# Kernel tuning notes

Measured on AMD Instinct MI355X. Metric: run time of the kernel, lower is better.

Reference implementation:

```python
import jax, jax.numpy as jnp
import numpy as np

B, P, N, E, H, D = 64, 256, 1000, 128, 8, 16
SQRT_E = 11.313708498984761  # sqrt(embedding_dim)
CLIP = 10.0                  # logit_clipping


def setup_inputs() -> dict:
    key = jax.random.key(0)
    ks = jax.random.split(key, 9)
    s = 0.05  # weight init scale
    return {
        "encoded_nodes": jax.random.normal(ks[0], (B, N, E), jnp.float32),
        "encoded_last_node": jax.random.normal(ks[1], (B, P, E), jnp.float32),
        "attr": jax.random.uniform(ks[2], (B, P, 1), jnp.float32),
        "ninf_mask": jnp.zeros((B, P, N), jnp.float32),
        # params stored [in, out] (apply as x @ W, equals torch Linear with W.T)
        "Wq_last": jax.random.normal(ks[3], (E + 1, H * D), jnp.float32) * s,
        "Wk": jax.random.normal(ks[4], (E, H * D), jnp.float32) * s,
        "Wv": jax.random.normal(ks[5], (E, H * D), jnp.float32) * s,
        "Wo": jax.random.normal(ks[6], (H * D, E), jnp.float32) * s,
        "bo": jax.random.normal(ks[7], (E,), jnp.float32) * s,
    }


def reference(encoded_nodes, encoded_last_node, attr, ninf_mask,
              Wq_last, Wk, Wv, Wo, bo):
    # set_kv: project encoded nodes to per-head K, V  -> [B, N, H, D]
    k = (encoded_nodes @ Wk).reshape(B, N, H, D)
    v = (encoded_nodes @ Wv).reshape(B, N, H, D)

    # query from (last node embedding, attr) -> [B, P, H, D]
    input_cat = jnp.concatenate([encoded_last_node, attr], axis=2)  # [B,P,E+1]
    q = (input_cat @ Wq_last).reshape(B, P, H, D)

    # multi-head attention with additive rank-3 -inf mask
    inv_sqrt_d = 1.0 / jnp.sqrt(jnp.float32(D))
    scores = jnp.einsum("bphd,bnhd->bhpn", q, k) * inv_sqrt_d
    scores = scores + ninf_mask[:, None, :, :]            # [B,H,P,N]
    weights = jax.nn.softmax(scores, axis=-1)
    out = jnp.einsum("bhpn,bnhd->bphd", weights, v).reshape(B, P, H * D)

    mh = out @ Wo + bo                                    # [B,P,E]

    # single-head tanh-clipped scoring against encoded nodes
    score = jnp.einsum("bpe,bne->bpn", mh, encoded_nodes) / SQRT_E
    score_masked = CLIP * jnp.tanh(score) + ninf_mask
    probs = jax.nn.softmax(score_masked, axis=2)          # [B,P,N]
    return probs
```

## Files before the change

kernel.cpp:

```cpp
#include <hip/hip_runtime.h>

#define BB 64
#define PP 256
#define NN 1000
#define NP 1024
#define EE 128
#define HH 8
#define DD 16

typedef __fp16 v4h __attribute__((ext_vector_type(4)));
typedef float v4f __attribute__((ext_vector_type(4)));


__global__ __launch_bounds__(256) void k1_qproj(const float* __restrict__ ln,
                                                const float* __restrict__ attr,
                                                const float* __restrict__ Wq,
                                                __fp16* __restrict__ Qh) {
    __shared__ __fp16 wt[128 * 132];
    __shared__ float attrs[64];
    const int tid = threadIdx.x;
    const int row0 = blockIdx.x * 64;
    for (int i = tid; i < 128 * 128; i += 256) {
        int k = i >> 7, n = i & 127;
        wt[n * 132 + k] = (__fp16)Wq[i];
    }
    if (tid < 64) attrs[tid] = attr[row0 + tid];
    __syncthreads();

    const int wid = tid >> 6, lane = tid & 63;
    const int lp = lane & 15, lg = lane >> 4;
    const int rb = row0 + wid * 16;

    const float* arow = ln + (size_t)(rb + lp) * 128;
    v4f acc[8];
#pragma unroll
    for (int cf = 0; cf < 8; cf++) acc[cf] = (v4f){0.f, 0.f, 0.f, 0.f};

#pragma unroll
    for (int k0 = 0; k0 < 8; k0++) {
        float4 av = *(const float4*)&arow[k0 * 16 + 4 * lg];
        v4h af;
        af[0] = (__fp16)av.x; af[1] = (__fp16)av.y;
        af[2] = (__fp16)av.z; af[3] = (__fp16)av.w;
#pragma unroll
        for (int cf = 0; cf < 8; cf++) {
            v4h bf = *(const v4h*)&wt[(cf * 16 + lp) * 132 + k0 * 16 + 4 * lg];
            acc[cf] = __builtin_amdgcn_mfma_f32_16x16x16f16(af, bf, acc[cf], 0, 0, 0);
        }
    }

#pragma unroll
    for (int cf = 0; cf < 8; cf++) {
        const int col = cf * 16 + lp;
        const float w128 = Wq[128 * 128 + col];
#pragma unroll
        for (int r = 0; r < 4; r++) {
            const int rl = wid * 16 + 4 * lg + r;
            float v = (acc[cf][r] + attrs[rl] * w128) * 0.25f;
            Qh[(size_t)(row0 + rl) * 128 + col] = (__fp16)v;
        }
    }
}

__global__ __launch_bounds__(256) void k2_kv(const float* __restrict__ nodes,
                                             const float* __restrict__ Wk,
                                             const float* __restrict__ Wv,
                                             __fp16* __restrict__ Kf,
                                             __fp16* __restrict__ Vt) {
    __shared__ __fp16 wt[128 * 132];
    const int tid = threadIdx.x;
    const int b = blockIdx.y;
    const int kv = blockIdx.z;
    const float* W = (kv == 0) ? Wk : Wv;
    for (int i = tid; i < 128 * 128; i += 256) {
        int k = i >> 7, n = i & 127;
        wt[n * 132 + k] = (__fp16)W[i];
    }
    __syncthreads();

    const int wid = tid >> 6, lane = tid & 63;
    const int lp = lane & 15, lg = lane >> 4;
    const int nb = blockIdx.x * 64 + wid * 16;

    int nr = nb + lp;
    if (nr >= NN) nr = NN - 1;
    const float* arow = nodes + (size_t)(b * NN + nr) * 128;

    v4f acc[8];
#pragma unroll
    for (int cf = 0; cf < 8; cf++) acc[cf] = (v4f){0.f, 0.f, 0.f, 0.f};

#pragma unroll
    for (int k0 = 0; k0 < 8; k0++) {
        float4 av = *(const float4*)&arow[k0 * 16 + 4 * lg];
        v4h af;
        af[0] = (__fp16)av.x; af[1] = (__fp16)av.y;
        af[2] = (__fp16)av.z; af[3] = (__fp16)av.w;
#pragma unroll
        for (int cf = 0; cf < 8; cf++) {
            v4h bf = *(const v4h*)&wt[(cf * 16 + lp) * 132 + k0 * 16 + 4 * lg];
            acc[cf] = __builtin_amdgcn_mfma_f32_16x16x16f16(af, bf, acc[cf], 0, 0, 0);
        }
    }

    if (kv == 0) {
#pragma unroll
        for (int cf = 0; cf < 8; cf++) {
            const size_t base = ((size_t)(b * HH + cf) << 14) + lp;
#pragma unroll
            for (int r = 0; r < 4; r++) {
                const int n = nb + 4 * lg + r;
                Kf[base + (size_t)n * 16] = (n < NN) ? (__fp16)acc[cf][r] : (__fp16)0.f;
            }
        }
    } else {
#pragma unroll
        for (int cf = 0; cf < 8; cf++) {
            v4h pk;
#pragma unroll
            for (int r = 0; r < 4; r++) {
                const int n = nb + 4 * lg + r;
                pk[r] = (n < NN) ? (__fp16)acc[cf][r] : (__fp16)0.f;
            }
            *(v4h*)&Vt[((size_t)(b * HH + cf) << 14) + (size_t)(nb >> 4) * 256 +
                       lp * 16 + 4 * lg] = pk;
        }
    }
}

__global__ __launch_bounds__(256) void k3_attn(const __fp16* __restrict__ Qh,
                                               const __fp16* __restrict__ Kf,
                                               const __fp16* __restrict__ Vt,
                                               const float* __restrict__ mask,
                                               __fp16* __restrict__ Aout) {
    __shared__ __fp16 sh[2][4][256];
    const int tid = threadIdx.x;
    const int bid = blockIdx.x;
    const int b = bid & 63;
    const int rest = bid >> 6;
    const int hg = rest & 3, pt = rest >> 2;
    const int h0 = hg * 2;
    const int p0 = pt * 64;

    const int wid = tid >> 6, lane = tid & 63;
    const int lp = lane & 15, lg = lane >> 4;
    const int pw = p0 + wid * 16;

    const __fp16* gsrc = ((wid < 2) ? Kf + ((size_t)(b * HH + h0 + wid) << 14)
                                    : Vt + ((size_t)(b * HH + h0 + wid - 2) << 14)) +
                         lane * 4;
    __fp16* sdst0 = &sh[0][wid][lane * 4];
    __fp16* sdst1 = &sh[1][wid][lane * 4];

    v4h qf[2];
    {
        const __fp16* qrow = Qh + (size_t)(b * PP + pw + lp) * 128 + h0 * 16 + 4 * lg;
        qf[0] = *(const v4h*)&qrow[0];
        qf[1] = *(const v4h*)&qrow[16];
    }

    const float* mrow = mask + (size_t)(b * PP + pw + lp) * NN;

    v4f acc[2];
    float lsum[2];
    acc[0] = (v4f){0.f, 0.f, 0.f, 0.f};
    acc[1] = (v4f){0.f, 0.f, 0.f, 0.f};
    lsum[0] = 0.f; lsum[1] = 0.f;
    const v4f zero4 = {0.f, 0.f, 0.f, 0.f};

    v4h st[2];
    float4 mv[2];
    st[0] = *(const v4h*)(gsrc);
    *(v4h*)sdst0 = st[0];
    st[1] = *(const v4h*)(gsrc + 256);
    mv[0] = *(const float4*)&mrow[4 * lg];
    __syncthreads();

#pragma unroll 2
    for (int s = 0; s < 62; s++) {
        const int p = s & 1;
        if (s + 2 <= 62) st[p] = *(const v4h*)(gsrc + (s + 2) * 256);
        {
            int moff = (s + 1) * 16 + 4 * lg;
            if (moff > 996) moff = 996;
            mv[p ^ 1] = *(const float4*)&mrow[moff];
        }

        v4h kf0 = *(const v4h*)&sh[p][0][lp * 16 + 4 * lg];
        v4h kf1 = *(const v4h*)&sh[p][1][lp * 16 + 4 * lg];
        v4h vf0 = *(const v4h*)&sh[p][2][lp * 16 + 4 * lg];
        v4h vf1 = *(const v4h*)&sh[p][3][lp * 16 + 4 * lg];
        const float4 m = mv[p];
        {
            v4f sc = __builtin_amdgcn_mfma_f32_16x16x16f16(kf0, qf[0], zero4, 0, 0, 0);
            float w0 = __expf(sc[0] + m.x);
            float w1 = __expf(sc[1] + m.y);
            float w2 = __expf(sc[2] + m.z);
            float w3 = __expf(sc[3] + m.w);
            lsum[0] += (w0 + w1) + (w2 + w3);
            v4h wf;
            wf[0] = (__fp16)w0; wf[1] = (__fp16)w1; wf[2] = (__fp16)w2; wf[3] = (__fp16)w3;
            acc[0] = __builtin_amdgcn_mfma_f32_16x16x16f16(wf, vf0, acc[0], 0, 0, 0);
        }
        {
            v4f sc = __builtin_amdgcn_mfma_f32_16x16x16f16(kf1, qf[1], zero4, 0, 0, 0);
            float w0 = __expf(sc[0] + m.x);
            float w1 = __expf(sc[1] + m.y);
            float w2 = __expf(sc[2] + m.z);
            float w3 = __expf(sc[3] + m.w);
            lsum[1] += (w0 + w1) + (w2 + w3);
            v4h wf;
            wf[0] = (__fp16)w0; wf[1] = (__fp16)w1; wf[2] = (__fp16)w2; wf[3] = (__fp16)w3;
            acc[1] = __builtin_amdgcn_mfma_f32_16x16x16f16(wf, vf1, acc[1], 0, 0, 0);
        }

        *(v4h*)((p == 0) ? sdst1 : sdst0) = st[p ^ 1];
        __syncthreads();
    }

    {
        const int nl = 992;
        const float4 m = mv[0];
        const bool c0 = (nl + 4 * lg + 0 < NN), c1 = (nl + 4 * lg + 1 < NN);
        const bool c2 = (nl + 4 * lg + 2 < NN), c3 = (nl + 4 * lg + 3 < NN);
        v4h kf0 = *(const v4h*)&sh[0][0][lp * 16 + 4 * lg];
        v4h kf1 = *(const v4h*)&sh[0][1][lp * 16 + 4 * lg];
        v4h vf0 = *(const v4h*)&sh[0][2][lp * 16 + 4 * lg];
        v4h vf1 = *(const v4h*)&sh[0][3][lp * 16 + 4 * lg];
        {
            v4f sc = __builtin_amdgcn_mfma_f32_16x16x16f16(kf0, qf[0], zero4, 0, 0, 0);
            float w0 = c0 ? __expf(sc[0] + m.x) : 0.f;
            float w1 = c1 ? __expf(sc[1] + m.y) : 0.f;
            float w2 = c2 ? __expf(sc[2] + m.z) : 0.f;
            float w3 = c3 ? __expf(sc[3] + m.w) : 0.f;
            lsum[0] += (w0 + w1) + (w2 + w3);
            v4h wf;
            wf[0] = (__fp16)w0; wf[1] = (__fp16)w1; wf[2] = (__fp16)w2; wf[3] = (__fp16)w3;
            acc[0] = __builtin_amdgcn_mfma_f32_16x16x16f16(wf, vf0, acc[0], 0, 0, 0);
        }
        {
            v4f sc = __builtin_amdgcn_mfma_f32_16x16x16f16(kf1, qf[1], zero4, 0, 0, 0);
            float w0 = c0 ? __expf(sc[0] + m.x) : 0.f;
            float w1 = c1 ? __expf(sc[1] + m.y) : 0.f;
            float w2 = c2 ? __expf(sc[2] + m.z) : 0.f;
            float w3 = c3 ? __expf(sc[3] + m.w) : 0.f;
            lsum[1] += (w0 + w1) + (w2 + w3);
            v4h wf;
            wf[0] = (__fp16)w0; wf[1] = (__fp16)w1; wf[2] = (__fp16)w2; wf[3] = (__fp16)w3;
            acc[1] = __builtin_amdgcn_mfma_f32_16x16x16f16(wf, vf1, acc[1], 0, 0, 0);
        }
    }

#pragma unroll
    for (int j = 0; j < 2; j++) {
        float l = lsum[j];
        l += __shfl_xor(l, 16);
        l += __shfl_xor(l, 32);
#pragma unroll
        for (int r = 0; r < 4; r++) {
            float denom = __shfl(l, 4 * lg + r);
            float inv = 1.f / denom;
            Aout[(size_t)(b * PP + pw + 4 * lg + r) * 128 + (h0 + j) * 16 + lp] =
                (__fp16)(acc[j][r] * inv);
        }
    }
}

__global__ __launch_bounds__(256) void k4_mh(const __fp16* __restrict__ Ain,
                                             const float* __restrict__ Wo,
                                             const float* __restrict__ bo,
                                             __fp16* __restrict__ Mh) {
    __shared__ __fp16 wt[128 * 132];
    const int tid = threadIdx.x;
    const int row0 = blockIdx.x * 64;
    for (int i = tid; i < 128 * 128; i += 256) {
        int k = i >> 7, n = i & 127;
        wt[n * 132 + k] = (__fp16)Wo[i];
    }
    __syncthreads();

    const int wid = tid >> 6, lane = tid & 63;
    const int lp = lane & 15, lg = lane >> 4;
    const int rb = row0 + wid * 16;

    const __fp16* arow = Ain + (size_t)(rb + lp) * 128;
    v4f acc[8];
#pragma unroll
    for (int cf = 0; cf < 8; cf++) acc[cf] = (v4f){0.f, 0.f, 0.f, 0.f};

#pragma unroll
    for (int k0 = 0; k0 < 8; k0++) {
        v4h af = *(const v4h*)&arow[k0 * 16 + 4 * lg];
#pragma unroll
        for (int cf = 0; cf < 8; cf++) {
            v4h bf = *(const v4h*)&wt[(cf * 16 + lp) * 132 + k0 * 16 + 4 * lg];
            acc[cf] = __builtin_amdgcn_mfma_f32_16x16x16f16(af, bf, acc[cf], 0, 0, 0);
        }
    }

    const float scale = 0.08838834764831845f;
#pragma unroll
    for (int cf = 0; cf < 8; cf++) {
        const int col = cf * 16 + lp;
        const float bb = bo[col];
#pragma unroll
        for (int r = 0; r < 4; r++) {
            const int rl = wid * 16 + 4 * lg + r;
            Mh[(size_t)(row0 + rl) * 128 + col] = (__fp16)((acc[cf][r] + bb) * scale);
        }
    }
}

__device__ __forceinline__ void k5_pref(int s, int wid, int lp, int lg,
                                        const float* __restrict__ nbase,
                                        float4 (&nb)[8]) {
    int nr = s * 128 + wid * 16 + lp;
    if (nr >= NN) nr = NN - 1;
    const float* a = nbase + (size_t)nr * 128 + 4 * lg;
#pragma unroll
    for (int ec = 0; ec < 8; ec++) nb[ec] = *(const float4*)&a[ec * 16];
}

__device__ __forceinline__ void k5_comp(int s, int wid, int lp, int lg,
                                        const v4h (&bf0)[8], const v4h (&bf1)[8],
                                        const float4 (&nb)[8],
                                        const float* __restrict__ mk0,
                                        const float* __restrict__ mk1,
                                        float& ls0, float& ls1,
                                        __fp16* __restrict__ probs) {
    const v4f zero4 = {0.f, 0.f, 0.f, 0.f};
    int mc = s * 128 + wid * 16 + 4 * lg;
    if (mc > 996) mc = 996;
    float4 m0 = *(const float4*)&mk0[mc];
    float4 m1 = *(const float4*)&mk1[mc];
    v4f a0 = zero4, a1 = zero4;
#pragma unroll
    for (int ec = 0; ec < 8; ec++) {
        float4 av = nb[ec];
        v4h af;
        af[0] = (__fp16)av.x; af[1] = (__fp16)av.y;
        af[2] = (__fp16)av.z; af[3] = (__fp16)av.w;
        a0 = __builtin_amdgcn_mfma_f32_16x16x16f16(af, bf0[ec], a0, 0, 0, 0);
        a1 = __builtin_amdgcn_mfma_f32_16x16x16f16(af, bf1[ec], a1, 0, 0, 0);
    }
    const int nt = s * 128 + wid * 16;
    const int nb4 = nt + 4 * lg;
#pragma unroll
    for (int t = 0; t < 2; t++) {
        const v4f ac = t ? a1 : a0;
        const float4 m = t ? m1 : m0;
        v4h wf;
        float ws = 0.f;
        if (nt + 15 < NN) {
            float e0 = __expf(2.f * ac[0]);
            float e1 = __expf(2.f * ac[1]);
            float e2 = __expf(2.f * ac[2]);
            float e3 = __expf(2.f * ac[3]);
            float w0 = __expf(fmaf(-20.f, __builtin_amdgcn_rcpf(e0 + 1.f), m.x));
            float w1 = __expf(fmaf(-20.f, __builtin_amdgcn_rcpf(e1 + 1.f), m.y));
            float w2 = __expf(fmaf(-20.f, __builtin_amdgcn_rcpf(e2 + 1.f), m.z));
            float w3 = __expf(fmaf(-20.f, __builtin_amdgcn_rcpf(e3 + 1.f), m.w));
            ws = (w0 + w1) + (w2 + w3);
            wf[0] = (__fp16)w0; wf[1] = (__fp16)w1; wf[2] = (__fp16)w2; wf[3] = (__fp16)w3;
        } else {
            float w0 = 0.f, w1 = 0.f, w2 = 0.f, w3 = 0.f;
            if (nb4 + 0 < NN) {
                float e = __expf(2.f * ac[0]);
                w0 = __expf(fmaf(-20.f, __builtin_amdgcn_rcpf(e + 1.f), m.x));
            }
            if (nb4 + 1 < NN) {
                float e = __expf(2.f * ac[1]);
                w1 = __expf(fmaf(-20.f, __builtin_amdgcn_rcpf(e + 1.f), m.y));
            }
            if (nb4 + 2 < NN) {
                float e = __expf(2.f * ac[2]);
                w2 = __expf(fmaf(-20.f, __builtin_amdgcn_rcpf(e + 1.f), m.z));
            }
            if (nb4 + 3 < NN) {
                float e = __expf(2.f * ac[3]);
                w3 = __expf(fmaf(-20.f, __builtin_amdgcn_rcpf(e + 1.f), m.w));
            }
            ws = (w0 + w1) + (w2 + w3);
            wf[0] = (__fp16)w0; wf[1] = (__fp16)w1; wf[2] = (__fp16)w2; wf[3] = (__fp16)w3;
        }
        if (t) ls1 += ws; else ls0 += ws;
        *(v4h*)&probs[(t * 16 + lp) * 1028 + nb4] = wf;
    }
}

__global__ __launch_bounds__(512, 4) void k5_final(const float* __restrict__ nodes,
                                                   const __fp16* __restrict__ Mh,
                                                   const float* __restrict__ mask,
                                                   float* __restrict__ out) {
    __shared__ __fp16 probs[32 * 1028];
    __shared__ float rowsum[32];
    __shared__ float rowinv[32];
    const int tid = threadIdx.x;
    const int bid = blockIdx.x;
    const int xcd = bid & 7;
    const int pt = (bid >> 3) & 7;
    const int b = ((bid >> 6) << 3) | xcd;
    const int p0 = pt * 32;

    if (tid < 32) rowsum[tid] = 0.f;

    const int wid = tid >> 6, lane = tid & 63;
    const int lp = lane & 15, lg = lane >> 4;

    v4h bf0[8], bf1[8];
    {
        const __fp16* mh0 = Mh + (size_t)(b * PP + p0 + lp) * 128;
        const __fp16* mh1 = mh0 + (size_t)16 * 128;
#pragma unroll
        for (int ec = 0; ec < 8; ec++) {
            bf0[ec] = *(const v4h*)&mh0[ec * 16 + 4 * lg];
            bf1[ec] = *(const v4h*)&mh1[ec * 16 + 4 * lg];
        }
    }
    __syncthreads();

    float ls0 = 0.f, ls1 = 0.f;
    const float* nbase = nodes + (size_t)b * NN * 128;
    const float* mk0 = mask + (size_t)(b * PP + p0 + lp) * NN;
    const float* mk1 = mk0 + (size_t)16 * NN;

    float4 nbA[8], nbB[8];
    k5_pref(0, wid, lp, lg, nbase, nbA);
    for (int s2 = 0; s2 < 4; s2++) {
        const int s = 2 * s2;
        k5_pref(s + 1, wid, lp, lg, nbase, nbB);
        k5_comp(s, wid, lp, lg, bf0, bf1, nbA, mk0, mk1, ls0, ls1, probs);
        if (s2 < 3) k5_pref(s + 2, wid, lp, lg, nbase, nbA);
        k5_comp(s + 1, wid, lp, lg, bf0, bf1, nbB, mk0, mk1, ls0, ls1, probs);
    }

    ls0 += __shfl_xor(ls0, 16);
    ls0 += __shfl_xor(ls0, 32);
    ls1 += __shfl_xor(ls1, 16);
    ls1 += __shfl_xor(ls1, 32);
    if (lane < 16) {
        atomicAdd(&rowsum[lane], ls0);
        atomicAdd(&rowsum[16 + lane], ls1);
    }
    __syncthreads();
    if (tid < 32) rowinv[tid] = 1.f / rowsum[tid];
    __syncthreads();

    if (tid < 500) {
        const int rg = tid / 250;
        const int c4 = (tid - rg * 250) * 4;
        const size_t obase = (size_t)(b * PP + p0 + rg * 16) * NN;
#pragma unroll 4
        for (int r = 0; r < 16; r++) {
            v4h pv = *(const v4h*)&probs[(rg * 16 + r) * 1028 + c4];
            float inv = rowinv[rg * 16 + r];
            float4 ov;
            ov.x = (float)pv[0] * inv;
            ov.y = (float)pv[1] * inv;
            ov.z = (float)pv[2] * inv;
            ov.w = (float)pv[3] * inv;
            *(float4*)&out[obase + (size_t)r * NN + c4] = ov;
        }
    }
}

extern "C" void kernel_launch(void* const* d_in, const int* in_sizes, int n_in,
                              void* d_out, int out_size, void* d_ws, size_t ws_size,
                              hipStream_t stream) {
    const float* nodes = (const float*)d_in[0];
    const float* ln    = (const float*)d_in[1];
    const float* attr  = (const float*)d_in[2];
    const float* mask  = (const float*)d_in[3];
    const float* Wq    = (const float*)d_in[4];
    const float* Wk    = (const float*)d_in[5];
    const float* Wv    = (const float*)d_in[6];
    const float* Wo    = (const float*)d_in[7];
    const float* bo    = (const float*)d_in[8];
    float* out = (float*)d_out;

    __fp16* AoutH = (__fp16*)d_ws;
    __fp16* Qh    = AoutH + 2097152;
    __fp16* Mhh   = Qh + 2097152;

    __fp16* Kf = (__fp16*)d_out;
    __fp16* Vt = Kf + (size_t)BB * HH * NP * 16;

    hipLaunchKernelGGL(k1_qproj, dim3(256), dim3(256), 0, stream, ln, attr, Wq, Qh);
    hipLaunchKernelGGL(k2_kv, dim3(16, 64, 2), dim3(256), 0, stream, nodes, Wk, Wv, Kf, Vt);
    hipLaunchKernelGGL(k3_attn, dim3(1024), dim3(256), 0, stream, Qh, Kf, Vt, mask, AoutH);
    hipLaunchKernelGGL(k4_mh, dim3(256), dim3(256), 0, stream, AoutH, Wo, bo, Mhh);
    hipLaunchKernelGGL(k5_final, dim3(512), dim3(512), 0, stream, nodes, Mhh, mask, out);
}
```

Before: 284.1 us.

## Restage K/V tiles in 32-key chunks with interleaved layout and wider loads

Changes the K and V global layouts written by the projection kernel to a 4-element interleaved tile order, so the attention kernel's shared-memory fragment reads become contiguous and bank-friendly. The attention loop now stages 32 keys per iteration with 8-wide fp16 loads, which halves the number of iterations and block barriers, and it prefetches two mask vectors per step. In exchange it doubles the shared-memory buffer and register use for staging, and it relies on the new index math staying consistent between the producer and consumer kernels and the tail step.

```diff
diff --git a/kernel.cpp b/kernel.cpp
--- a/kernel.cpp
+++ b/kernel.cpp
@@ -9,6 +9,7 @@
 #define DD 16
 
 typedef __fp16 v4h __attribute__((ext_vector_type(4)));
+typedef __fp16 v8h __attribute__((ext_vector_type(8)));
 typedef float v4f __attribute__((ext_vector_type(4)));
 
 
@@ -106,11 +107,12 @@
     if (kv == 0) {
 #pragma unroll
         for (int cf = 0; cf < 8; cf++) {
-            const size_t base = ((size_t)(b * HH + cf) << 14) + lp;
+            const size_t base = ((size_t)(b * HH + cf) << 14) +
+                                (size_t)(nb >> 4) * 256 + (lp >> 2) * 64 + (lp & 3);
 #pragma unroll
             for (int r = 0; r < 4; r++) {
                 const int n = nb + 4 * lg + r;
-                Kf[base + (size_t)n * 16] = (n < NN) ? (__fp16)acc[cf][r] : (__fp16)0.f;
+                Kf[base + (4 * lg + r) * 4] = (n < NN) ? (__fp16)acc[cf][r] : (__fp16)0.f;
             }
         }
     } else {
@@ -123,7 +125,7 @@
                 pk[r] = (n < NN) ? (__fp16)acc[cf][r] : (__fp16)0.f;
             }
             *(v4h*)&Vt[((size_t)(b * HH + cf) << 14) + (size_t)(nb >> 4) * 256 +
-                       lp * 16 + 4 * lg] = pk;
+                       lg * 64 + lp * 4] = pk;
         }
     }
 }
@@ -133,7 +135,7 @@
                                                const __fp16* __restrict__ Vt,
                                                const float* __restrict__ mask,
                                                __fp16* __restrict__ Aout) {
-    __shared__ __fp16 sh[2][4][256];
+    __shared__ __fp16 sh[2][4][512];
     const int tid = threadIdx.x;
     const int bid = blockIdx.x;
     const int b = bid & 63;
@@ -148,9 +150,7 @@
 
     const __fp16* gsrc = ((wid < 2) ? Kf + ((size_t)(b * HH + h0 + wid) << 14)
                                     : Vt + ((size_t)(b * HH + h0 + wid - 2) << 14)) +
-                         lane * 4;
-    __fp16* sdst0 = &sh[0][wid][lane * 4];
-    __fp16* sdst1 = &sh[1][wid][lane * 4];
+                         lane * 8;
 
     v4h qf[2];
     {
@@ -168,65 +168,73 @@
     lsum[0] = 0.f; lsum[1] = 0.f;
     const v4f zero4 = {0.f, 0.f, 0.f, 0.f};
 
-    v4h st[2];
-    float4 mv[2];
-    st[0] = *(const v4h*)(gsrc);
-    *(v4h*)sdst0 = st[0];
-    st[1] = *(const v4h*)(gsrc + 256);
-    mv[0] = *(const float4*)&mrow[4 * lg];
+    v8h st[2];
+    float4 mv[2][2];
+    st[0] = *(const v8h*)(gsrc);
+    *(v8h*)&sh[0][wid][lane * 8] = st[0];
+    st[1] = *(const v8h*)(gsrc + 512);
+    mv[0][0] = *(const float4*)&mrow[4 * lg];
+    mv[0][1] = *(const float4*)&mrow[16 + 4 * lg];
     __syncthreads();
 
 #pragma unroll 2
-    for (int s = 0; s < 62; s++) {
+    for (int s = 0; s < 31; s++) {
         const int p = s & 1;
-        if (s + 2 <= 62) st[p] = *(const v4h*)(gsrc + (s + 2) * 256);
+        if (s < 30) st[p] = *(const v8h*)(gsrc + (s + 2) * 512);
         {
-            int moff = (s + 1) * 16 + 4 * lg;
-            if (moff > 996) moff = 996;
-            mv[p ^ 1] = *(const float4*)&mrow[moff];
-        }
-
-        v4h kf0 = *(const v4h*)&sh[p][0][lp * 16 + 4 * lg];
-        v4h kf1 = *(const v4h*)&sh[p][1][lp * 16 + 4 * lg];
-        v4h vf0 = *(const v4h*)&sh[p][2][lp * 16 + 4 * lg];
-        v4h vf1 = *(const v4h*)&sh[p][3][lp * 16 + 4 * lg];
-        const float4 m = mv[p];
-        {
-            v4f sc = __builtin_amdgcn_mfma_f32_16x16x16f16(kf0, qf[0], zero4, 0, 0, 0);
-            float w0 = __expf(sc[0] + m.x);
-            float w1 = __expf(sc[1] + m.y);
-            float w2 = __expf(sc[2] + m.z);
-            float w3 = __expf(sc[3] + m.w);
-            lsum[0] += (w0 + w1) + (w2 + w3);
-            v4h wf;
-            wf[0] = (__fp16)w0; wf[1] = (__fp16)w1; wf[2] = (__fp16)w2; wf[3] = (__fp16)w3;
-            acc[0] = __builtin_amdgcn_mfma_f32_16x16x16f16(wf, vf0, acc[0], 0, 0, 0);
-        }
-        {
-            v4f sc = __builtin_amdgcn_mfma_f32_16x16x16f16(kf1, qf[1], zero4, 0, 0, 0);
-            float w0 = __expf(sc[0] + m.x);
-            float w1 = __expf(sc[1] + m.y);
-            float w2 = __expf(sc[2] + m.z);
-            float w3 = __expf(sc[3] + m.w);
-            lsum[1] += (w0 + w1) + (w2 + w3);
-            v4h wf;
-            wf[0] = (__fp16)w0; wf[1] = (__fp16)w1; wf[2] = (__fp16)w2; wf[3] = (__fp16)w3;
-            acc[1] = __builtin_amdgcn_mfma_f32_16x16x16f16(wf, vf1, acc[1], 0, 0, 0);
-        }
-
-        *(v4h*)((p == 0) ? sdst1 : sdst0) = st[p ^ 1];
+            int c0 = (s + 1) * 32 + 4 * lg;
+            int c1 = c0 + 16;
+            if (c0 > 996) c0 = 996;
+            if (c1 > 996) c1 = 996;
+            mv[p ^ 1][0] = *(const float4*)&mrow[c0];
+            mv[p ^ 1][1] = *(const float4*)&mrow[c1];
+        }
+
+#pragma unroll
+        for (int u = 0; u < 2; u++) {
+            const int off = u * 256 + 64 * lg + 4 * lp;
+            v4h kf0 = *(const v4h*)&sh[p][0][off];
+            v4h kf1 = *(const v4h*)&sh[p][1][off];
+            v4h vf0 = *(const v4h*)&sh[p][2][off];
+            v4h vf1 = *(const v4h*)&sh[p][3][off];
+            const float4 m = mv[p][u];
+            {
+                v4f sc = __builtin_amdgcn_mfma_f32_16x16x16f16(kf0, qf[0], zero4, 0, 0, 0);
+                float w0 = __expf(sc[0] + m.x);
+                float w1 = __expf(sc[1] + m.y);
+                float w2 = __expf(sc[2] + m.z);
+                float w3 = __expf(sc[3] + m.w);
+                lsum[0] += (w0 + w1) + (w2 + w3);
+                v4h wf;
+                wf[0] = (__fp16)w0; wf[1] = (__fp16)w1; wf[2] = (__fp16)w2; wf[3] = (__fp16)w3;
+                acc[0] = __builtin_amdgcn_mfma_f32_16x16x16f16(wf, vf0, acc[0], 0, 0, 0);
+            }
+            {
+                v4f sc = __builtin_amdgcn_mfma_f32_16x16x16f16(kf1, qf[1], zero4, 0, 0, 0);
+                float w0 = __expf(sc[0] + m.x);
+                float w1 = __expf(sc[1] + m.y);
+                float w2 = __expf(sc[2] + m.z);
+                float w3 = __expf(sc[3] + m.w);
+                lsum[1] += (w0 + w1) + (w2 + w3);
+                v4h wf;
+                wf[0] = (__fp16)w0; wf[1] = (__fp16)w1; wf[2] = (__fp16)w2; wf[3] = (__fp16)w3;
+                acc[1] = __builtin_amdgcn_mfma_f32_16x16x16f16(wf, vf1, acc[1], 0, 0, 0);
+            }
+        }
+
+        *(v8h*)&sh[p ^ 1][wid][lane * 8] = st[p ^ 1];
         __syncthreads();
     }
 
     {
-        const int nl = 992;
-        const float4 m = mv[0];
-        const bool c0 = (nl + 4 * lg + 0 < NN), c1 = (nl + 4 * lg + 1 < NN);
-        const bool c2 = (nl + 4 * lg + 2 < NN), c3 = (nl + 4 * lg + 3 < NN);
-        v4h kf0 = *(const v4h*)&sh[0][0][lp * 16 + 4 * lg];
-        v4h kf1 = *(const v4h*)&sh[0][1][lp * 16 + 4 * lg];
-        v4h vf0 = *(const v4h*)&sh[0][2][lp * 16 + 4 * lg];
-        v4h vf1 = *(const v4h*)&sh[0][3][lp * 16 + 4 * lg];
+        const float4 m = mv[1][0];
+        const bool c0 = (992 + 4 * lg + 0 < NN), c1 = (992 + 4 * lg + 1 < NN);
+        const bool c2 = (992 + 4 * lg + 2 < NN), c3 = (992 + 4 * lg + 3 < NN);
+        const int off = 64 * lg + 4 * lp;
+        v4h kf0 = *(const v4h*)&sh[1][0][off];
+        v4h kf1 = *(const v4h*)&sh[1][1][off];
+        v4h vf0 = *(const v4h*)&sh[1][2][off];
+        v4h vf1 = *(const v4h*)&sh[1][3][off];
         {
             v4f sc = __builtin_amdgcn_mfma_f32_16x16x16f16(kf0, qf[0], zero4, 0, 0, 0);
             float w0 = c0 ? __expf(sc[0] + m.x) : 0.f;
```

After: 343.5 us. +20.9%, slower.
